# Kernel optimization log

Hardware: AMD Instinct MI355X
Metric: run time of the kernel (lower is better)

The kernel has to match this reference:

```python
import jax, jax.numpy as jnp
import numpy as np

D_MODEL = 1024
BATCH = 16
SEQ = 1024
RATIO = 2.0 / 3.0  # layer_idx=2, n_layers=4
THRESH = 0.5


def _layer_norm(x, gamma, beta, eps=1e-5):
    mu = jnp.mean(x, axis=-1, keepdims=True)
    var = jnp.var(x, axis=-1, keepdims=True)
    return (x - mu) * jax.lax.rsqrt(var + eps) * gamma + beta


def _ternary(x):
    # FixedThresholdTernarySpike(threshold=0.5): sign(x) if |x|>0.5 else 0
    return jnp.where(x > THRESH, 1.0, jnp.where(x < -THRESH, -1.0, 0.0)).astype(x.dtype)


def setup_inputs() -> dict:
    key = jax.random.key(0)
    ks = jax.random.split(key, 10)
    scale = 0.1 / np.sqrt(D_MODEL)
    x = jax.random.normal(ks[0], (BATCH, SEQ, D_MODEL), dtype=jnp.float32)
    S0 = jnp.zeros((BATCH, D_MODEL), dtype=jnp.float32)
    mix_init = 1.0 - RATIO
    return {
        "x": x,
        "S0": S0,
        "ln_gamma": jnp.ones((D_MODEL,), jnp.float32),
        "ln_beta": jnp.zeros((D_MODEL,), jnp.float32),
        "time_mix_k": jnp.full((D_MODEL,), mix_init, jnp.float32) + 0.02 * jax.random.normal(ks[1], (D_MODEL,)),
        "time_mix_v": jnp.full((D_MODEL,), mix_init, jnp.float32) + 0.02 * jax.random.normal(ks[2], (D_MODEL,)),
        "time_mix_r": jnp.full((D_MODEL,), mix_init, jnp.float32) + 0.02 * jax.random.normal(ks[3], (D_MODEL,)),
        "decay_weight": jnp.full((D_MODEL,), -0.5, jnp.float32) + 0.02 * jax.random.normal(ks[4], (D_MODEL,)),
        "Wk": scale * jax.random.normal(ks[5], (D_MODEL, D_MODEL), jnp.float32),
        "Wv": scale * jax.random.normal(ks[6], (D_MODEL, D_MODEL), jnp.float32),
        "Wr": scale * jax.random.normal(ks[7], (D_MODEL, D_MODEL), jnp.float32),
        "Wo": scale * jax.random.normal(ks[8], (D_MODEL, D_MODEL), jnp.float32),
    }


def reference(x, S0, ln_gamma, ln_beta, time_mix_k, time_mix_v, time_mix_r,
              decay_weight, Wk, Wv, Wr, Wo):
    # x: (B, T, D)
    x_norm = _layer_norm(x, ln_gamma, ln_beta)                       # LN applied to every step
    # prev_x at t is LN(x[t-1]); at t=0 it is zeros (module uses zeros_like, not LN of zeros)
    prev_norm = jnp.concatenate([jnp.zeros_like(x_norm[:, :1]), x_norm[:, :-1]], axis=1)

    xk = x_norm * time_mix_k + prev_norm * (1.0 - time_mix_k)
    xv = x_norm * time_mix_v + prev_norm * (1.0 - time_mix_v)
    xr = x_norm * time_mix_r + prev_norm * (1.0 - time_mix_r)

    k = _ternary(jnp.einsum('btd,ed->bte', xk, Wk))                  # ternary spikes
    v = _ternary(jnp.einsum('btd,ed->bte', xv, Wv))
    r = jax.nn.sigmoid(jnp.einsum('btd,ed->bte', xr, Wr))

    decay = jax.nn.sigmoid(decay_weight)                             # (D,)
    kv = k * v                                                       # (B, T, D)

    def step(S, kv_t):                                               # S: (B, D)
        S_new = decay * S + kv_t
        return S_new, S_new

    S_final, S_all = jax.lax.scan(step, S0, jnp.swapaxes(kv, 0, 1))  # S_all: (T, B, D)
    S_all = jnp.swapaxes(S_all, 0, 1)                                # (B, T, D)

    out = x + r * jnp.einsum('btd,ed->bte', S_all, Wo)
    return out, S_final
```

## Files before the change

kernel.cpp:

```cpp
#include <hip/hip_runtime.h>
#include <hip/hip_bf16.h>
#include <math.h>

#define D_MODEL 1024
#define SEQ 1024
#define BATCH 16
#define NROWS (BATCH * SEQ)
#define KT8 8

typedef float f32x4 __attribute__((ext_vector_type(4)));
typedef int   i32x4 __attribute__((ext_vector_type(4)));
typedef int   i32x8 __attribute__((ext_vector_type(8)));
typedef __bf16 bf16x4 __attribute__((ext_vector_type(4)));
typedef __hip_bfloat16 bf16;
typedef unsigned char u8;

__device__ __forceinline__ float bf2f(bf16 v) { return __bfloat162float(v); }
__device__ __forceinline__ bf16 f2bf(float v) { return __float2bfloat16(v); }

__device__ __forceinline__ void gload_lds16(const u8* g, u8* l) {
    __builtin_amdgcn_global_load_lds(
        (const __attribute__((address_space(1))) void*)g,
        (__attribute__((address_space(3))) void*)l, 16, 0, 0);
}

__device__ __forceinline__ int pk_fp8x4(float a, float b, float c, float d) {
    int r = __builtin_amdgcn_cvt_pk_fp8_f32(a, b, 0, false);
    r = __builtin_amdgcn_cvt_pk_fp8_f32(c, d, r, true);
    return r;
}

__device__ __forceinline__ void tile_coords128(int lin, int& m0, int& n0) {
    const int xcd = lin & 7;
    const int loc = lin >> 3;
    m0 = (xcd * 16 + (loc & 15)) * 128;
    n0 = (loc >> 4) * 128;
}

__global__ void conv_w4_kernel(const float* __restrict__ s0, const float* __restrict__ s1,
                               const float* __restrict__ s2, const float* __restrict__ s3,
                               u8* __restrict__ dst) {
    const float* srcs[4] = {s0, s1, s2, s3};
    const float* src = srcs[blockIdx.y];
    int* d = reinterpret_cast<int*>(dst + (size_t)blockIdx.y * (D_MODEL * D_MODEL));
    int i = blockIdx.x * blockDim.x + threadIdx.x;
    const int stride = gridDim.x * blockDim.x;
    for (; i < (D_MODEL * D_MODEL) / 4; i += stride) {
        float4 f = reinterpret_cast<const float4*>(src)[i];
        d[i] = pk_fp8x4(f.x, f.y, f.z, f.w);
    }
}

__global__ __launch_bounds__(256) void lnmix_kernel(
    const float* __restrict__ x, const float* __restrict__ gamma, const float* __restrict__ beta,
    const float* __restrict__ tmk, const float* __restrict__ tmv, const float* __restrict__ tmr,
    u8* __restrict__ xk, u8* __restrict__ xv, u8* __restrict__ xr)
{
    const int wave = threadIdx.x >> 6, lane = threadIdx.x & 63;
    const int lb = (blockIdx.x & 7) * (gridDim.x >> 3) + (blockIdx.x >> 3);
    const int row = lb * 4 + wave;
    const int t = row & (SEQ - 1);
    const size_t base = (size_t)row * D_MODEL;

    float4 vc[4], vp[4];
    float sc = 0.f, sc2 = 0.f, sp = 0.f, sp2 = 0.f;
#pragma unroll
    for (int c = 0; c < 4; c++) {
        const int d = lane * 4 + c * 256;
        vc[c] = *reinterpret_cast<const float4*>(x + base + d);
        if (t == 0) { vp[c] = make_float4(0.f, 0.f, 0.f, 0.f); }
        else        { vp[c] = *reinterpret_cast<const float4*>(x + base - D_MODEL + d); }
        sc  += vc[c].x + vc[c].y + vc[c].z + vc[c].w;
        sc2 += vc[c].x * vc[c].x + vc[c].y * vc[c].y + vc[c].z * vc[c].z + vc[c].w * vc[c].w;
        sp  += vp[c].x + vp[c].y + vp[c].z + vp[c].w;
        sp2 += vp[c].x * vp[c].x + vp[c].y * vp[c].y + vp[c].z * vp[c].z + vp[c].w * vp[c].w;
    }
#pragma unroll
    for (int off = 1; off < 64; off <<= 1) {
        sc  += __shfl_xor(sc, off);
        sc2 += __shfl_xor(sc2, off);
        sp  += __shfl_xor(sp, off);
        sp2 += __shfl_xor(sp2, off);
    }
    const float muc = sc * (1.0f / D_MODEL);
    const float rc  = rsqrtf(sc2 * (1.0f / D_MODEL) - muc * muc + 1e-5f);
    const float mup = sp * (1.0f / D_MODEL);
    const float rp  = rsqrtf(sp2 * (1.0f / D_MODEL) - mup * mup + 1e-5f);

#pragma unroll
    for (int c = 0; c < 4; c++) {
        const int d = lane * 4 + c * 256;
        float4 g  = *reinterpret_cast<const float4*>(gamma + d);
        float4 b  = *reinterpret_cast<const float4*>(beta + d);
        float4 mk = *reinterpret_cast<const float4*>(tmk + d);
        float4 mv = *reinterpret_cast<const float4*>(tmv + d);
        float4 mr = *reinterpret_cast<const float4*>(tmr + d);
        float cn[4], pn[4];
        cn[0] = (vc[c].x - muc) * rc * g.x + b.x;
        cn[1] = (vc[c].y - muc) * rc * g.y + b.y;
        cn[2] = (vc[c].z - muc) * rc * g.z + b.z;
        cn[3] = (vc[c].w - muc) * rc * g.w + b.w;
        if (t == 0) { pn[0] = pn[1] = pn[2] = pn[3] = 0.f; }
        else {
            pn[0] = (vp[c].x - mup) * rp * g.x + b.x;
            pn[1] = (vp[c].y - mup) * rp * g.y + b.y;
            pn[2] = (vp[c].z - mup) * rp * g.z + b.z;
            pn[3] = (vp[c].w - mup) * rp * g.w + b.w;
        }
        const float mkv[4] = {mk.x, mk.y, mk.z, mk.w};
        const float mvv[4] = {mv.x, mv.y, mv.z, mv.w};
        const float mrv[4] = {mr.x, mr.y, mr.z, mr.w};
        float ok[4], ov[4], orr[4];
#pragma unroll
        for (int e = 0; e < 4; e++) {
            ok[e]  = mkv[e] * cn[e] + (1.0f - mkv[e]) * pn[e];
            ov[e]  = mvv[e] * cn[e] + (1.0f - mvv[e]) * pn[e];
            orr[e] = mrv[e] * cn[e] + (1.0f - mrv[e]) * pn[e];
        }
        *reinterpret_cast<int*>(xk + base + d) = pk_fp8x4(ok[0], ok[1], ok[2], ok[3]);
        *reinterpret_cast<int*>(xv + base + d) = pk_fp8x4(ov[0], ov[1], ov[2], ov[3]);
        *reinterpret_cast<int*>(xr + base + d) = pk_fp8x4(orr[0], orr[1], orr[2], orr[3]);
    }
}

__device__ __forceinline__ void gemm128_fp8_core(
    const u8* __restrict__ A, const u8* __restrict__ W,
    u8* __restrict__ As, u8* __restrict__ Bs,
    int m0, int n0, f32x4 (&acc)[4][4])
{
    const int tid  = threadIdx.x;
    const int wave = tid >> 6, lane = tid & 63;
    const int wm = wave >> 1, wn = wave & 1;
    const int mf = lane & 15, quad = lane >> 4;
    const int srow = tid >> 3;
    const int sw = ((tid & 7) ^ (srow & 7)) * 16;

    const u8* Ag = A + (size_t)(m0 + srow) * D_MODEL + sw;
    const u8* Bg = W + (size_t)(n0 + srow) * D_MODEL + sw;

    const int swz0 = ((2 * quad)     ^ (mf & 7)) * 16;
    const int swz1 = ((2 * quad + 1) ^ (mf & 7)) * 16;
    const u8* aB0 = As + (wm * 64 + mf) * 128 + swz0;
    const u8* aB1 = As + (wm * 64 + mf) * 128 + swz1;
    const u8* bB0 = Bs + (wn * 64 + mf) * 128 + swz0;
    const u8* bB1 = Bs + (wn * 64 + mf) * 128 + swz1;

#pragma unroll 1
    for (int kt = 0; kt < KT8; ++kt) {
        __syncthreads();
#pragma unroll
        for (int g = 0; g < 4; ++g) {
            gload_lds16(Ag + (size_t)g * 32 * D_MODEL + kt * 128, As + g * 4096 + wave * 1024);
            gload_lds16(Bg + (size_t)g * 32 * D_MODEL + kt * 128, Bs + g * 4096 + wave * 1024);
        }
        __syncthreads();

        i32x8 af[4], bf[4];
#pragma unroll
        for (int i = 0; i < 4; ++i) {
            i32x4 lo = *reinterpret_cast<const i32x4*>(aB0 + i * 2048);
            i32x4 hi = *reinterpret_cast<const i32x4*>(aB1 + i * 2048);
            af[i] = __builtin_shufflevector(lo, hi, 0, 1, 2, 3, 4, 5, 6, 7);
        }
#pragma unroll
        for (int j = 0; j < 4; ++j) {
            i32x4 lo = *reinterpret_cast<const i32x4*>(bB0 + j * 2048);
            i32x4 hi = *reinterpret_cast<const i32x4*>(bB1 + j * 2048);
            bf[j] = __builtin_shufflevector(lo, hi, 0, 1, 2, 3, 4, 5, 6, 7);
        }
#pragma unroll
        for (int i = 0; i < 4; ++i)
#pragma unroll
            for (int j = 0; j < 4; ++j)
                acc[i][j] = __builtin_amdgcn_mfma_scale_f32_16x16x128_f8f6f4(
                    af[i], bf[j], acc[i][j], 0, 0, 0, 127, 0, 127);
    }
}

__global__ __launch_bounds__(256) void gemm128_kv(
    const u8* __restrict__ A0, const u8* __restrict__ A1,
    const u8* __restrict__ W0, const u8* __restrict__ W1,
    char* __restrict__ O0, char* __restrict__ O1)
{
    const u8* A = blockIdx.y ? A1 : A0;
    const u8* W = blockIdx.y ? W1 : W0;
    char* O     = blockIdx.y ? O1 : O0;

    __shared__ __align__(16) u8 As[16384];
    __shared__ __align__(16) u8 Bs[16384];
    int m0, n0;
    tile_coords128(blockIdx.x, m0, n0);

    f32x4 acc[4][4] = {};
    gemm128_fp8_core(A, W, As, Bs, m0, n0, acc);

    const int lane = threadIdx.x & 63, wave = threadIdx.x >> 6;
    const int wm = wave >> 1, wn = wave & 1;
    const int mf = lane & 15, quad = lane >> 4;
#pragma unroll
    for (int i = 0; i < 4; ++i)
#pragma unroll
        for (int j = 0; j < 4; ++j)
#pragma unroll
            for (int e = 0; e < 4; ++e) {
                const int row = m0 + wm * 64 + i * 16 + quad * 4 + e;
                const int col = n0 + wn * 64 + j * 16 + mf;
                const float v = acc[i][j][e];
                O[(size_t)row * D_MODEL + col] = (v > 0.5f) ? 1 : ((v < -0.5f) ? -1 : 0);
            }
}

__global__ __launch_bounds__(256) void rscan_kernel(
    const u8* __restrict__ XR, const u8* __restrict__ WrB, bf16* __restrict__ RB,
    const char* __restrict__ K8, const char* __restrict__ V8,
    const float* __restrict__ dw, const float* __restrict__ S0,
    u8* __restrict__ sall, float* __restrict__ sfinal)
{
    __shared__ __align__(16) u8 smem[32768];

    if (blockIdx.x >= 256) {
        u8* As = smem;
        u8* Bs = smem + 16384;
        int m0, n0;
        tile_coords128(blockIdx.x - 256, m0, n0);

        f32x4 acc[4][4] = {};
        gemm128_fp8_core(XR, WrB, As, Bs, m0, n0, acc);

        const int lane = threadIdx.x & 63, wave = threadIdx.x >> 6;
        const int wm = wave >> 1, wn = wave & 1;
        const int mf = lane & 15, quad = lane >> 4;
#pragma unroll
        for (int i = 0; i < 4; ++i)
#pragma unroll
            for (int j = 0; j < 4; ++j)
#pragma unroll
                for (int e = 0; e < 4; ++e) {
                    const int row = m0 + wm * 64 + i * 16 + quad * 4 + e;
                    const int col = n0 + wn * 64 + j * 16 + mf;
                    RB[(size_t)row * D_MODEL + col] = f2bf(1.0f / (1.0f + __expf(-acc[i][j][e])));
                }
        return;
    }

    unsigned int* kvp = reinterpret_cast<unsigned int*>(smem);
    float* Lf = reinterpret_cast<float*>(smem + 16384);
    float* P  = reinterpret_cast<float*>(smem + 16384 + 1024);

    const int bid = blockIdx.x;
    const int db  = bid & 15, b = bid >> 4;
    const int ch  = threadIdx.x & 63;
    const int q   = threadIdx.x >> 6;
    const int d   = db * 64 + ch;

    const float dec = 1.0f / (1.0f + __expf(-dw[d]));
    float c256 = dec;
#pragma unroll
    for (int i = 0; i < 8; i++) c256 *= c256;

    const size_t base = ((size_t)b * SEQ + q * 256) * D_MODEL + d;

    float S = 0.f;
    size_t idx = base;
    unsigned int w = 0;
    for (int t = 0; t < 256; t += 4, idx += 4 * D_MODEL) {
        const int k0 = K8[idx];
        const int v0 = V8[idx];
        const int k1 = K8[idx + 1 * D_MODEL];
        const int v1 = V8[idx + 1 * D_MODEL];
        const int k2 = K8[idx + 2 * D_MODEL];
        const int v2 = V8[idx + 2 * D_MODEL];
        const int k3 = K8[idx + 3 * D_MODEL];
        const int v3 = V8[idx + 3 * D_MODEL];
        const int p0 = k0 * v0, p1 = k1 * v1, p2 = k2 * v2, p3 = k3 * v3;
        S = dec * S + (float)p0;
        S = dec * S + (float)p1;
        S = dec * S + (float)p2;
        S = dec * S + (float)p3;
        const int sh = 2 * (t & 15);
        w |= ((unsigned int)(p0 + 1) << sh) | ((unsigned int)(p1 + 1) << (sh + 2)) |
             ((unsigned int)(p2 + 1) << (sh + 4)) | ((unsigned int)(p3 + 1) << (sh + 6));
        if ((t & 15) == 12) { kvp[(q * 16 + (t >> 4)) * 64 + ch] = w; w = 0; }
    }

    Lf[q * 64 + ch] = S;
    __syncthreads();
    if (q == 0) {
        float p = S0[b * D_MODEL + d];
        P[ch] = p;
        p = Lf[0 * 64 + ch] + c256 * p; P[1 * 64 + ch] = p;
        p = Lf[1 * 64 + ch] + c256 * p; P[2 * 64 + ch] = p;
        p = Lf[2 * 64 + ch] + c256 * p; P[3 * 64 + ch] = p;
        p = Lf[3 * 64 + ch] + c256 * p;
        sfinal[b * D_MODEL + d] = p;
    }
    __syncthreads();

    float Sv = P[q * 64 + ch];
    idx = base;
    for (int t16 = 0; t16 < 16; ++t16) {
        const unsigned int pw = kvp[(q * 16 + t16) * 64 + ch];
#pragma unroll
        for (int j = 0; j < 16; ++j, idx += D_MODEL) {
            const float p = (float)((int)((pw >> (2 * j)) & 3) - 1);
            Sv = dec * Sv + p;
            const int enc = __builtin_amdgcn_cvt_pk_fp8_f32(Sv, 0.f, 0, false);
            sall[idx] = (u8)(enc & 255);
        }
    }
}

__global__ __launch_bounds__(256) void gemm128_out(
    const u8* __restrict__ SA, const u8* __restrict__ Wo,
    const bf16* __restrict__ R, const float* __restrict__ x, float* __restrict__ out)
{
    __shared__ __align__(16) u8 As[16384];
    __shared__ __align__(16) u8 Bs[16384];
    int m0, n0;
    tile_coords128(blockIdx.x, m0, n0);

    f32x4 acc[4][4] = {};
    gemm128_fp8_core(SA, Wo, As, Bs, m0, n0, acc);

    const int lane = threadIdx.x & 63, wave = threadIdx.x >> 6;
    const int wm = wave >> 1, wn = wave & 1;
    const int mf = lane & 15, quad = lane >> 4;
#pragma unroll
    for (int i = 0; i < 4; ++i)
#pragma unroll
        for (int j = 0; j < 4; ++j)
#pragma unroll
            for (int e = 0; e < 4; ++e) {
                const int row = m0 + wm * 64 + i * 16 + quad * 4 + e;
                const int col = n0 + wn * 64 + j * 16 + mf;
                const size_t o = (size_t)row * D_MODEL + col;
                out[o] = x[o] + bf2f(R[o]) * acc[i][j][e];
            }
}

extern "C" void kernel_launch(void* const* d_in, const int* in_sizes, int n_in,
                              void* d_out, int out_size, void* d_ws, size_t ws_size,
                              hipStream_t stream) {
    const float* x     = (const float*)d_in[0];
    const float* S0    = (const float*)d_in[1];
    const float* gamma = (const float*)d_in[2];
    const float* beta  = (const float*)d_in[3];
    const float* tmk   = (const float*)d_in[4];
    const float* tmv   = (const float*)d_in[5];
    const float* tmr   = (const float*)d_in[6];
    const float* dw    = (const float*)d_in[7];
    const float* Wk    = (const float*)d_in[8];
    const float* Wv    = (const float*)d_in[9];
    const float* Wr    = (const float*)d_in[10];
    const float* Wo    = (const float*)d_in[11];
    float* out = (float*)d_out;

    const int WN = D_MODEL * D_MODEL;
    const size_t MATN = (size_t)NROWS * D_MODEL;

    u8* ws   = (u8*)d_ws;
    u8* Wk8  = ws;
    u8* Wv8  = Wk8 + WN;
    u8* Wr8  = Wv8 + WN;
    u8* Wo8  = Wr8 + WN;
    u8* XK8  = Wo8 + WN;
    u8* XV8  = XK8 + MATN;
    u8* XR8  = XV8 + MATN;
    char* Kt8 = (char*)(XR8 + MATN);
    char* Vt8 = Kt8 + MATN;
    u8* SA8  = (u8*)(Vt8 + MATN);
    bf16* RB = (bf16*)(SA8 + MATN);

    conv_w4_kernel<<<dim3(256, 4), 256, 0, stream>>>(Wk, Wv, Wr, Wo, ws);

    lnmix_kernel<<<NROWS / 4, 256, 0, stream>>>(x, gamma, beta, tmk, tmv, tmr, XK8, XV8, XR8);

    gemm128_kv<<<dim3(1024, 2), 256, 0, stream>>>(XK8, XV8, Wk8, Wv8, Kt8, Vt8);

    rscan_kernel<<<1280, 256, 0, stream>>>(XR8, Wr8, RB, Kt8, Vt8, dw, S0, SA8, out + MATN);

    gemm128_out<<<1024, 256, 0, stream>>>(SA8, Wo8, RB, x, out);
}
```

Measured before the change: 282.3 us.

## Fuse receptance GEMM into output GEMM and widen scan chunking

The Wr projection and sigmoid move out of the scan kernel into the output GEMM, which now runs both GEMMs per tile and applies r from registers. This removes the bf16 R buffer write and its read-back. The scan kernel now uses 512 threads with 8 chunks of 128 steps per channel group for more parallelism in the recurrence. The LDS swizzle mapping is also changed to alter how the MFMA operand reads hit banks. The trade-off is that the scan kernel can no longer overlap with the R GEMM, and the output kernel carries two accumulator sets, which raises register pressure.

```diff
diff --git a/kernel.cpp b/kernel.cpp
--- a/kernel.cpp
+++ b/kernel.cpp
@@ -11,7 +11,6 @@
 typedef float f32x4 __attribute__((ext_vector_type(4)));
 typedef int   i32x4 __attribute__((ext_vector_type(4)));
 typedef int   i32x8 __attribute__((ext_vector_type(8)));
-typedef __bf16 bf16x4 __attribute__((ext_vector_type(4)));
 typedef __hip_bfloat16 bf16;
 typedef unsigned char u8;
 
@@ -133,13 +132,14 @@
     const int wm = wave >> 1, wn = wave & 1;
     const int mf = lane & 15, quad = lane >> 4;
     const int srow = tid >> 3;
-    const int sw = ((tid & 7) ^ (srow & 7)) * 16;
+    const int u  = (tid & 7) ^ (srow & 7);
+    const int sw = (((u & 3) << 1) | (u >> 2)) * 16;
 
     const u8* Ag = A + (size_t)(m0 + srow) * D_MODEL + sw;
     const u8* Bg = W + (size_t)(n0 + srow) * D_MODEL + sw;
 
-    const int swz0 = ((2 * quad)     ^ (mf & 7)) * 16;
-    const int swz1 = ((2 * quad + 1) ^ (mf & 7)) * 16;
+    const int swz0 = ((quad)     ^ (mf & 7)) * 16;
+    const int swz1 = ((4 + quad) ^ (mf & 7)) * 16;
     const u8* aB0 = As + (wm * 64 + mf) * 128 + swz0;
     const u8* aB1 = As + (wm * 64 + mf) * 128 + swz1;
     const u8* bB0 = Bs + (wn * 64 + mf) * 128 + swz0;
@@ -210,42 +210,14 @@
             }
 }
 
-__global__ __launch_bounds__(256) void rscan_kernel(
-    const u8* __restrict__ XR, const u8* __restrict__ WrB, bf16* __restrict__ RB,
+__global__ __launch_bounds__(512) void scan_kernel(
     const char* __restrict__ K8, const char* __restrict__ V8,
     const float* __restrict__ dw, const float* __restrict__ S0,
     u8* __restrict__ sall, float* __restrict__ sfinal)
 {
-    __shared__ __align__(16) u8 smem[32768];
-
-    if (blockIdx.x >= 256) {
-        u8* As = smem;
-        u8* Bs = smem + 16384;
-        int m0, n0;
-        tile_coords128(blockIdx.x - 256, m0, n0);
-
-        f32x4 acc[4][4] = {};
-        gemm128_fp8_core(XR, WrB, As, Bs, m0, n0, acc);
-
-        const int lane = threadIdx.x & 63, wave = threadIdx.x >> 6;
-        const int wm = wave >> 1, wn = wave & 1;
-        const int mf = lane & 15, quad = lane >> 4;
-#pragma unroll
-        for (int i = 0; i < 4; ++i)
-#pragma unroll
-            for (int j = 0; j < 4; ++j)
-#pragma unroll
-                for (int e = 0; e < 4; ++e) {
-                    const int row = m0 + wm * 64 + i * 16 + quad * 4 + e;
-                    const int col = n0 + wn * 64 + j * 16 + mf;
-                    RB[(size_t)row * D_MODEL + col] = f2bf(1.0f / (1.0f + __expf(-acc[i][j][e])));
-                }
-        return;
-    }
-
-    unsigned int* kvp = reinterpret_cast<unsigned int*>(smem);
-    float* Lf = reinterpret_cast<float*>(smem + 16384);
-    float* P  = reinterpret_cast<float*>(smem + 16384 + 1024);
+    __shared__ unsigned int kvp[8][8][64];
+    __shared__ float Lf[8][64];
+    __shared__ float P[8][64];
 
     const int bid = blockIdx.x;
     const int db  = bid & 15, b = bid >> 4;
@@ -254,16 +226,16 @@
     const int d   = db * 64 + ch;
 
     const float dec = 1.0f / (1.0f + __expf(-dw[d]));
-    float c256 = dec;
-#pragma unroll
-    for (int i = 0; i < 8; i++) c256 *= c256;
-
-    const size_t base = ((size_t)b * SEQ + q * 256) * D_MODEL + d;
+    float c128 = dec;
+#pragma unroll
+    for (int i = 0; i < 7; i++) c128 *= c128;
+
+    const size_t base = ((size_t)b * SEQ + q * 128) * D_MODEL + d;
 
     float S = 0.f;
     size_t idx = base;
     unsigned int w = 0;
-    for (int t = 0; t < 256; t += 4, idx += 4 * D_MODEL) {
+    for (int t = 0; t < 128; t += 4, idx += 4 * D_MODEL) {
         const int k0 = K8[idx];
         const int v0 = V8[idx];
         const int k1 = K8[idx + 1 * D_MODEL];
@@ -280,26 +252,28 @@
         const int sh = 2 * (t & 15);
         w |= ((unsigned int)(p0 + 1) << sh) | ((unsigned int)(p1 + 1) << (sh + 2)) |
              ((unsigned int)(p2 + 1) << (sh + 4)) | ((unsigned int)(p3 + 1) << (sh + 6));
-        if ((t & 15) == 12) { kvp[(q * 16 + (t >> 4)) * 64 + ch] = w; w = 0; }
-    }
-
-    Lf[q * 64 + ch] = S;
+        if ((t & 15) == 12) { kvp[q][t >> 4][ch] = w; w = 0; }
+    }
+
+    Lf[q][ch] = S;
     __syncthreads();
     if (q == 0) {
         float p = S0[b * D_MODEL + d];
-        P[ch] = p;
-        p = Lf[0 * 64 + ch] + c256 * p; P[1 * 64 + ch] = p;
-        p = Lf[1 * 64 + ch] + c256 * p; P[2 * 64 + ch] = p;
-        p = Lf[2 * 64 + ch] + c256 * p; P[3 * 64 + ch] = p;
-        p = Lf[3 * 64 + ch] + c256 * p;
+        P[0][ch] = p;
+#pragma unroll
+        for (int j = 1; j < 8; ++j) {
+            p = Lf[j - 1][ch] + c128 * p;
+            P[j][ch] = p;
+        }
+        p = Lf[7][ch] + c128 * p;
         sfinal[b * D_MODEL + d] = p;
     }
     __syncthreads();
 
-    float Sv = P[q * 64 + ch];
+    float Sv = P[q][ch];
     idx = base;
-    for (int t16 = 0; t16 < 16; ++t16) {
-        const unsigned int pw = kvp[(q * 16 + t16) * 64 + ch];
+    for (int t16 = 0; t16 < 8; ++t16) {
+        const unsigned int pw = kvp[q][t16][ch];
 #pragma unroll
         for (int j = 0; j < 16; ++j, idx += D_MODEL) {
             const float p = (float)((int)((pw >> (2 * j)) & 3) - 1);
@@ -310,15 +284,26 @@
     }
 }
 
-__global__ __launch_bounds__(256) void gemm128_out(
+__global__ __launch_bounds__(256, 2) void gemm128_outR(
+    const u8* __restrict__ XR, const u8* __restrict__ Wr,
     const u8* __restrict__ SA, const u8* __restrict__ Wo,
-    const bf16* __restrict__ R, const float* __restrict__ x, float* __restrict__ out)
+    const float* __restrict__ x, float* __restrict__ out)
 {
     __shared__ __align__(16) u8 As[16384];
     __shared__ __align__(16) u8 Bs[16384];
     int m0, n0;
     tile_coords128(blockIdx.x, m0, n0);
 
+    f32x4 accR[4][4] = {};
+    gemm128_fp8_core(XR, Wr, As, Bs, m0, n0, accR);
+#pragma unroll
+    for (int i = 0; i < 4; ++i)
+#pragma unroll
+        for (int j = 0; j < 4; ++j)
+#pragma unroll
+            for (int e = 0; e < 4; ++e)
+                accR[i][j][e] = 1.0f / (1.0f + __expf(-accR[i][j][e]));
+
     f32x4 acc[4][4] = {};
     gemm128_fp8_core(SA, Wo, As, Bs, m0, n0, acc);
 
@@ -334,7 +319,7 @@
                 const int row = m0 + wm * 64 + i * 16 + quad * 4 + e;
                 const int col = n0 + wn * 64 + j * 16 + mf;
                 const size_t o = (size_t)row * D_MODEL + col;
-                out[o] = x[o] + bf2f(R[o]) * acc[i][j][e];
+                out[o] = x[o] + accR[i][j][e] * acc[i][j][e];
             }
 }
 
@@ -369,7 +354,6 @@
     char* Kt8 = (char*)(XR8 + MATN);
     char* Vt8 = Kt8 + MATN;
     u8* SA8  = (u8*)(Vt8 + MATN);
-    bf16* RB = (bf16*)(SA8 + MATN);
 
     conv_w4_kernel<<<dim3(256, 4), 256, 0, stream>>>(Wk, Wv, Wr, Wo, ws);
 
@@ -377,7 +361,7 @@
 
     gemm128_kv<<<dim3(1024, 2), 256, 0, stream>>>(XK8, XV8, Wk8, Wv8, Kt8, Vt8);
 
-    rscan_kernel<<<1280, 256, 0, stream>>>(XR8, Wr8, RB, Kt8, Vt8, dw, S0, SA8, out + MATN);
-
-    gemm128_out<<<1024, 256, 0, stream>>>(SA8, Wo8, RB, x, out);
-}
+    scan_kernel<<<256, 512, 0, stream>>>(Kt8, Vt8, dw, S0, SA8, out + MATN);
+
+    gemm128_outR<<<1024, 256, 0, stream>>>(XR8, Wr8, SA8, Wo8, x, out);
+}
```

Result: faster. 270.2 us (-4.3%).
